# Performance work log

Hardware: AMD Instinct MI355X
Metric: run time of the kernel (lower is better)

The kernel has to match this reference:

```python
import jax, jax.numpy as jnp
import numpy as np

N_NODES = 50000
N_EDGES = 600000
N_FEAT = 64
D = 128
N_GRAPHS = 1024
N_LAYERS = 4


def setup_inputs() -> dict:
    key = jax.random.key(0)
    ks = jax.random.split(key, 16)
    x = jax.random.normal(ks[0], (N_NODES, N_FEAT), dtype=jnp.float32)
    edge_index = jax.random.randint(ks[1], (2, N_EDGES), 0, N_NODES, dtype=jnp.int64)
    batch_index = jnp.sort(jax.random.randint(ks[2], (N_NODES,), 0, N_GRAPHS, dtype=jnp.int64))
    def lin(k, fan_in, fan_out):
        s = 1.0 / np.sqrt(fan_in)
        kw, kb = jax.random.split(k)
        w = jax.random.uniform(kw, (fan_in, fan_out), minval=-s, maxval=s, dtype=jnp.float32)
        b = jax.random.uniform(kb, (fan_out,), minval=-s, maxval=s, dtype=jnp.float32)
        return w, b
    w0, b0 = lin(ks[3], N_FEAT, D)
    w1, b1 = lin(ks[4], D, D)
    w2, b2 = lin(ks[5], D, D)
    w3, b3 = lin(ks[6], D, D)
    wp, bp = lin(ks[7], D, D)
    return {"x": x, "edge_index": edge_index, "batch_index": batch_index,
            "w0": w0, "b0": b0, "w1": w1, "b1": b1, "w2": w2, "b2": b2,
            "w3": w3, "b3": b3, "wp": wp, "bp": bp}


def _gin_layer(x, src, dst, w, b):
    # GINConv with eps=0: MLP(x_i + sum_{j in N(i)} x_j); MLP = Linear -> ReLU
    agg = jax.ops.segment_sum(x[src], dst, num_segments=N_NODES)
    return jax.nn.relu((x + agg) @ w + b)


def reference(x, edge_index, batch_index, w0, b0, w1, b1, w2, b2, w3, b3, wp, bp):
    src, dst = edge_index[0], edge_index[1]
    # first layer changes width 64 -> 128; agg happens in input width
    agg0 = jax.ops.segment_sum(x[src], dst, num_segments=N_NODES)
    h = jax.nn.relu((x + agg0) @ w0 + b0)
    for w, b in ((w1, b1), (w2, b2), (w3, b3)):
        h = _gin_layer(h, src, dst, w, b)
    # global mean pool per graph
    sums = jax.ops.segment_sum(h, batch_index, num_segments=N_GRAPHS)
    counts = jax.ops.segment_sum(jnp.ones((N_NODES,), dtype=h.dtype), batch_index, num_segments=N_GRAPHS)
    pooled = sums / jnp.maximum(counts, 1.0)[:, None]
    # post_mp: Linear -> ReLU (dropout identity at inference)
    return jax.nn.relu(pooled @ wp + bp)
```

## Files before the change

kernel.cpp:

```cpp
#include <hip/hip_runtime.h>
#include <hip/hip_fp16.h>


#define N_NODES  50000
#define N_EDGES  600000
#define N_FEAT   64
#define DIM      128
#define N_GRAPHS 1024
#define NB_SCAN  49

typedef _Float16 f16x8 __attribute__((ext_vector_type(8)));
typedef float    f32x4 __attribute__((ext_vector_type(4)));

__global__ __launch_bounds__(256) void hist_k(
    const int* __restrict__ dst, int* __restrict__ cnt) {
  int e = blockIdx.x * 256 + threadIdx.x;
  if (e < N_EDGES) atomicAdd(&cnt[dst[e]], 1);
}

__global__ __launch_bounds__(256) void scan_part_k(
    const int* __restrict__ cnt, int* __restrict__ part) {
  __shared__ int ws[4];
  int t = threadIdx.x, b = blockIdx.x;
  int base = b * 1024 + t * 4;
  int s = 0;
  if (base + 3 < N_NODES) {
    int4 v = *reinterpret_cast<const int4*>(cnt + base);
    s = v.x + v.y + v.z + v.w;
  } else {
    for (int i = 0; i < 4; ++i) if (base + i < N_NODES) s += cnt[base + i];
  }
  for (int off = 32; off; off >>= 1) s += __shfl_down(s, off, 64);
  int lane = t & 63, wv = t >> 6;
  if (lane == 0) ws[wv] = s;
  __syncthreads();
  if (t == 0) part[b] = ws[0] + ws[1] + ws[2] + ws[3];
}

__global__ __launch_bounds__(256) void scan_write_k(
    const int* __restrict__ cnt, const int* __restrict__ part,
    int* __restrict__ row_ptr, int* __restrict__ fill) {
  __shared__ int wsum[4];
  __shared__ int blk_off_s;
  int t = threadIdx.x, b = blockIdx.x;
  int lane = t & 63, wv = t >> 6;
  int base = b * 1024 + t * 4;

  if (base + 3 < N_NODES)
    *reinterpret_cast<int4*>(fill + base) = make_int4(0, 0, 0, 0);
  else
    for (int i = 0; i < 4; ++i) if (base + i < N_NODES) fill[base + i] = 0;

  if (t < 64) {
    int v = (t < NB_SCAN) ? part[t] : 0;
    int incl = v;
    for (int off = 1; off < 64; off <<= 1) {
      int u = __shfl_up(incl, off, 64);
      if (t >= off) incl += u;
    }
    if (t == b) blk_off_s = incl - v;
  }

  int v[4];
#pragma unroll
  for (int i = 0; i < 4; ++i) v[i] = (base + i < N_NODES) ? cnt[base + i] : 0;
  int ls = v[0] + v[1] + v[2] + v[3];
  int incl = ls;
  for (int off = 1; off < 64; off <<= 1) {
    int u = __shfl_up(incl, off, 64);
    if (lane >= off) incl += u;
  }
  if (lane == 63) wsum[wv] = incl;
  __syncthreads();
  int woff = 0;
  for (int w = 0; w < wv; ++w) woff += wsum[w];
  int off0 = blk_off_s + woff + (incl - ls);
  int rp0 = off0, rp1 = off0 + v[0], rp2 = rp1 + v[1], rp3 = rp2 + v[2];
  if (base + 3 < N_NODES)
    *reinterpret_cast<int4*>(row_ptr + base) = make_int4(rp0, rp1, rp2, rp3);
  else {
    int rp[4] = {rp0, rp1, rp2, rp3};
    for (int i = 0; i < 4; ++i) if (base + i < N_NODES) row_ptr[base + i] = rp[i];
  }
  if (b == 0 && t == 0) row_ptr[N_NODES] = N_EDGES;
}

__global__ __launch_bounds__(256) void fill_k(
    const int* __restrict__ src, const int* __restrict__ dst,
    const int* __restrict__ row_ptr, int* __restrict__ fill,
    int* __restrict__ csr_src) {
  int e = blockIdx.x * 256 + threadIdx.x;
  if (e >= N_EDGES) return;
  int d = dst[e];
  int pos = row_ptr[d] + atomicAdd(&fill[d], 1);
  csr_src[pos] = src[e];
}

#define CNTZ  (N_NODES / 4)
#define XWORK (N_NODES * N_FEAT / 4)
__global__ __launch_bounds__(256) void prep_k(
    const float* __restrict__ x, __half* __restrict__ xh,
    const float* __restrict__ w0, const float* __restrict__ w1,
    const float* __restrict__ w2, const float* __restrict__ w3,
    __half* __restrict__ Wt0, __half* __restrict__ Wt1,
    __half* __restrict__ Wt2, __half* __restrict__ Wt3,
    int* __restrict__ cnt) {
  int i = blockIdx.x * 256 + threadIdx.x;
  if (i < CNTZ) {
    *reinterpret_cast<int4*>(cnt + i * 4) = make_int4(0, 0, 0, 0);
    return;
  }
  i -= CNTZ;
  if (i < XWORK) {
    float4 v = *reinterpret_cast<const float4*>(x + (size_t)i * 4);
    union { __half2 h2[2]; uint2 u; } pk;
    pk.h2[0] = __floats2half2_rn(v.x, v.y);
    pk.h2[1] = __floats2half2_rn(v.z, v.w);
    *reinterpret_cast<uint2*>(xh + (size_t)i * 4) = pk.u;
    return;
  }
  int j = i - XWORK;
  if (j < N_FEAT * DIM) {
    int k = j >> 7, n = j & 127;
    Wt0[n * N_FEAT + k] = __float2half(w0[j]);
    return;
  }
  j -= N_FEAT * DIM;
  if (j >= 3 * DIM * DIM) return;
  int wsel = j / (DIM * DIM);
  int jj = j - wsel * (DIM * DIM);
  int k = jj >> 7, n = jj & 127;
  const float* W = (wsel == 0) ? w1 : (wsel == 1) ? w2 : w3;
  __half* Wt     = (wsel == 0) ? Wt1 : (wsel == 1) ? Wt2 : Wt3;
  Wt[n * DIM + k] = __float2half(W[jj]);
}

template<int K, bool EPI>
__global__ __launch_bounds__(256) void mfma_gemm_k(
    const __half* __restrict__ A, const __half* __restrict__ Wt,
    const float* __restrict__ bias, __half* __restrict__ y, int M) {
  constexpr int KP = K + 8;
  constexpr int OSP = 128 + 16;
  constexpr size_t STAGE = (size_t)(64 + 128) * KP * sizeof(__half);
  constexpr size_t OUTSZ = (size_t)64 * OSP * sizeof(__half);
  __shared__ __align__(16) char smem[STAGE > OUTSZ ? STAGE : OUTSZ];
  __half (*As)[KP]  = reinterpret_cast<__half(*)[KP]>(smem);
  __half (*Ws)[KP]  = reinterpret_cast<__half(*)[KP]>(smem + (size_t)64 * KP * sizeof(__half));
  __half (*Os)[OSP] = reinterpret_cast<__half(*)[OSP]>(smem);

  int tid = threadIdx.x;
  int row0 = blockIdx.x * 64;

  for (int i = tid; i < 64 * (K / 8); i += 256) {
    int r = i / (K / 8), c = (i % (K / 8)) * 8;
    int row = row0 + r;
    f16x8 v = {};
    if (row < M) v = *reinterpret_cast<const f16x8*>(A + (size_t)row * K + c);
    *reinterpret_cast<f16x8*>(&As[r][c]) = v;
  }
  for (int i = tid; i < 128 * (K / 8); i += 256) {
    int r = i / (K / 8), c = (i % (K / 8)) * 8;
    *reinterpret_cast<f16x8*>(&Ws[r][c]) =
        *reinterpret_cast<const f16x8*>(Wt + (size_t)r * K + c);
  }
  __syncthreads();

  int w = tid >> 6, lane = tid & 63;
  int quad = lane >> 4, m = lane & 15;

  f32x4 acc[8];
#pragma unroll
  for (int t = 0; t < 8; ++t) acc[t] = (f32x4){0.f, 0.f, 0.f, 0.f};

#pragma unroll
  for (int kk = 0; kk < K; kk += 32) {
    f16x8 a = *reinterpret_cast<const f16x8*>(&As[w * 16 + m][kk + quad * 8]);
#pragma unroll
    for (int t = 0; t < 8; ++t) {
      f16x8 b = *reinterpret_cast<const f16x8*>(&Ws[t * 16 + m][kk + quad * 8]);
      acc[t] = __builtin_amdgcn_mfma_f32_16x16x32_f16(a, b, acc[t], 0, 0, 0);
    }
  }

  __syncthreads();

#pragma unroll
  for (int t = 0; t < 8; ++t) {
    float bv = EPI ? bias[t * 16 + m] : 0.f;
#pragma unroll
    for (int r = 0; r < 4; ++r) {
      float v = acc[t][r];
      if (EPI) v = fmaxf(v + bv, 0.f);
      Os[w * 16 + quad * 4 + r][t * 16 + m] = __float2half(v);
    }
  }
  __syncthreads();

#pragma unroll
  for (int it = 0; it < 4; ++it) {
    int i = tid + it * 256;
    int r = i >> 4, c = (i & 15) * 8;
    int row = row0 + r;
    if (row < M)
      *reinterpret_cast<f16x8*>(y + (size_t)row * 128 + c) =
          *reinterpret_cast<const f16x8*>(&Os[r][c]);
  }
}

template<int F, bool BR>
__global__ __launch_bounds__(256) void gather_k(
    const __half* __restrict__ y, const int* __restrict__ row_ptr,
    const int* __restrict__ csr_src, const float* __restrict__ bias,
    __half* __restrict__ hout) {
  constexpr int CH = F / 8;
  const f16x8* yv = reinterpret_cast<const f16x8*>(y);
  int gid  = blockIdx.x * 256 + threadIdx.x;
  int node = gid / CH;
  int l    = gid % CH;
  if (node >= N_NODES) return;
  int beg = row_ptr[node], end = row_ptr[node + 1];

  f16x8 self = yv[(size_t)node * CH + l];
  float acc[8];
#pragma unroll
  for (int v = 0; v < 8; ++v) acc[v] = (float)self[v];

  int e = beg;
  for (; e + 3 < end; e += 4) {
    int s0 = csr_src[e+0], s1 = csr_src[e+1], s2 = csr_src[e+2], s3 = csr_src[e+3];
    f16x8 v0 = yv[(size_t)s0 * CH + l];
    f16x8 v1 = yv[(size_t)s1 * CH + l];
    f16x8 v2 = yv[(size_t)s2 * CH + l];
    f16x8 v3 = yv[(size_t)s3 * CH + l];
#pragma unroll
    for (int v = 0; v < 8; ++v)
      acc[v] += ((float)v0[v] + (float)v1[v]) + ((float)v2[v] + (float)v3[v]);
  }
  for (; e < end; ++e) {
    f16x8 v0 = yv[(size_t)csr_src[e] * CH + l];
#pragma unroll
    for (int v = 0; v < 8; ++v) acc[v] += (float)v0[v];
  }

  f16x8 o;
  if (BR) {
    float4 b0 = *reinterpret_cast<const float4*>(bias + l * 8);
    float4 b1 = *reinterpret_cast<const float4*>(bias + l * 8 + 4);
    float bb[8] = {b0.x, b0.y, b0.z, b0.w, b1.x, b1.y, b1.z, b1.w};
#pragma unroll
    for (int v = 0; v < 8; ++v) o[v] = (_Float16)fmaxf(acc[v] + bb[v], 0.f);
  } else {
#pragma unroll
    for (int v = 0; v < 8; ++v) o[v] = (_Float16)acc[v];
  }
  reinterpret_cast<f16x8*>(hout)[(size_t)node * CH + l] = o;
}

__global__ __launch_bounds__(128) void pool_post_k(
    const __half* __restrict__ h, const int* __restrict__ batch,
    const float* __restrict__ W, const float* __restrict__ bias,
    float* __restrict__ out) {
  __shared__ float xs[DIM];
  int g = blockIdx.x;
  int col = threadIdx.x;
  int lo = 0, hi = N_NODES;
  while (lo < hi) { int mid = (lo + hi) >> 1; if (batch[mid] < g) lo = mid + 1; else hi = mid; }
  int beg = lo;
  hi = N_NODES;
  while (lo < hi) { int mid = (lo + hi) >> 1; if (batch[mid] < g + 1) lo = mid + 1; else hi = mid; }
  int end = lo;

  float acc = 0.f;
  for (int n = beg; n < end; ++n) acc += __half2float(h[(size_t)n * DIM + col]);
  float cnt = fmaxf((float)(end - beg), 1.0f);
  xs[col] = acc / cnt;
  __syncthreads();
  float o = bias[col];
  for (int k = 0; k < DIM; ++k)
    o = fmaf(xs[k], W[(size_t)k * DIM + col], o);
  out[(size_t)g * DIM + col] = fmaxf(o, 0.f);
}

extern "C" void kernel_launch(void* const* d_in, const int* in_sizes, int n_in,
                              void* d_out, int out_size, void* d_ws, size_t ws_size,
                              hipStream_t stream) {
  const float* x    = (const float*)d_in[0];
  const int*   ei   = (const int*)d_in[1];
  const int*   batch= (const int*)d_in[2];
  const float* w0 = (const float*)d_in[3];  const float* b0 = (const float*)d_in[4];
  const float* w1 = (const float*)d_in[5];  const float* b1 = (const float*)d_in[6];
  const float* w2 = (const float*)d_in[7];  const float* b2 = (const float*)d_in[8];
  const float* w3 = (const float*)d_in[9];  const float* b3 = (const float*)d_in[10];
  const float* wp = (const float*)d_in[11]; const float* bp = (const float*)d_in[12];
  float* out = (float*)d_out;

  const int* src = ei;
  const int* dst = ei + N_EDGES;

  __half* xh = (__half*)d_ws;
  __half* y  = xh + (size_t)N_NODES * N_FEAT;
  __half* h  = y  + (size_t)N_NODES * DIM;
  __half* Wt0 = h + (size_t)N_NODES * DIM;
  __half* Wt1 = Wt0 + N_FEAT * DIM;
  __half* Wt2 = Wt1 + DIM * DIM;
  __half* Wt3 = Wt2 + DIM * DIM;
  int* cnt     = (int*)(Wt3 + DIM * DIM);
  int* fill    = cnt + N_NODES;
  int* part    = fill + N_NODES;
  int* row_ptr = part + 64;
  int* csr_src = row_ptr + (N_NODES + 1);
  __half* s = y;

  {
    int total = CNTZ + XWORK + N_FEAT * DIM + 3 * DIM * DIM;
    prep_k<<<(total + 255) / 256, 256, 0, stream>>>(x, xh, w0, w1, w2, w3,
                                                    Wt0, Wt1, Wt2, Wt3, cnt);
  }
  hist_k<<<(N_EDGES + 255) / 256, 256, 0, stream>>>(dst, cnt);
  scan_part_k <<<NB_SCAN, 256, 0, stream>>>(cnt, part);
  scan_write_k<<<NB_SCAN, 256, 0, stream>>>(cnt, part, row_ptr, fill);
  fill_k<<<(N_EDGES + 255) / 256, 256, 0, stream>>>(src, dst, row_ptr, fill, csr_src);

  int mgrid = (N_NODES + 63) / 64;

  gather_k<N_FEAT, false><<<(N_NODES * (N_FEAT/8) + 255) / 256, 256, 0, stream>>>(
      xh, row_ptr, csr_src, nullptr, s);
  mfma_gemm_k<N_FEAT, true><<<mgrid, 256, 0, stream>>>(s, Wt0, b0, h, N_NODES);

  const __half* Wl[3] = {Wt1, Wt2, Wt3};
  const float*  Bl[3] = {b1, b2, b3};
  for (int l = 0; l < 3; ++l) {
    mfma_gemm_k<DIM, false><<<mgrid, 256, 0, stream>>>(h, Wl[l], nullptr, y, N_NODES);
    gather_k<DIM, true><<<(N_NODES * (DIM/8) + 255) / 256, 256, 0, stream>>>(
        y, row_ptr, csr_src, Bl[l], h);
  }

  pool_post_k<<<N_GRAPHS, 128, 0, stream>>>(h, batch, wp, bp, out);
}
```

Measured before the change: 311.7 us.

## Fuse all GNN stages into one persistent cooperative kernel with grid syncs

Replaces the chain of about fifteen separate kernel launches with a single cooperative persistent kernel of 512 blocks that runs each stage as a grid-stride phase, separated by grid-wide barriers, to remove launch overhead and inter-kernel gaps. The GEMM is also retiled to 128-row tiles, with A fragments held in registers and two MFMA row-slabs per wave. A multi-kernel fallback path is kept for devices that cannot do cooperative launch. The cost is limited parallelism per phase (a fixed 512-block grid) and grid.sync overhead, and the pool phase now runs on 256-thread blocks with half the threads idle.

```diff
diff --git a/kernel.cpp b/kernel.cpp
--- a/kernel.cpp
+++ b/kernel.cpp
@@ -1,5 +1,8 @@
 #include <hip/hip_runtime.h>
 #include <hip/hip_fp16.h>
+#include <hip/hip_cooperative_groups.h>
+
+namespace cg = cooperative_groups;
 
 
 #define N_NODES  50000
@@ -8,62 +11,113 @@
 #define DIM      128
 #define N_GRAPHS 1024
 #define NB_SCAN  49
+#define GRID     512
+#define TPB      256
+#define GT128    ((N_NODES + 127) / 128)
+#define SMEM_BYTES 36864
 
 typedef _Float16 f16x8 __attribute__((ext_vector_type(8)));
 typedef float    f32x4 __attribute__((ext_vector_type(4)));
 
-__global__ __launch_bounds__(256) void hist_k(
-    const int* __restrict__ dst, int* __restrict__ cnt) {
-  int e = blockIdx.x * 256 + threadIdx.x;
-  if (e < N_EDGES) atomicAdd(&cnt[dst[e]], 1);
-}
-
-__global__ __launch_bounds__(256) void scan_part_k(
-    const int* __restrict__ cnt, int* __restrict__ part) {
-  __shared__ int ws[4];
-  int t = threadIdx.x, b = blockIdx.x;
+#define CNTZ  (N_NODES / 4)
+#define XWORK (N_NODES * N_FEAT / 4)
+#define PREP_TOTAL (CNTZ + XWORK + N_FEAT * DIM + 3 * DIM * DIM)
+
+struct Params {
+  const float* x; const int* src; const int* dst; const int* batch;
+  const float *w0, *b0, *w1, *b1, *w2, *b2, *w3, *b3, *wp, *bp;
+  float* out;
+  __half *xh, *y, *h, *Wt0, *Wt1, *Wt2, *Wt3;
+  int *cnt, *fill, *part, *row_ptr, *csr_src;
+};
+
+
+__device__ __forceinline__ void prep_phase(const Params& p) {
+  for (int i0 = blockIdx.x * TPB + threadIdx.x; i0 < PREP_TOTAL;
+       i0 += gridDim.x * TPB) {
+    int i = i0;
+    if (i < CNTZ) {
+      *reinterpret_cast<int4*>(p.cnt + i * 4) = make_int4(0, 0, 0, 0);
+      continue;
+    }
+    i -= CNTZ;
+    if (i < XWORK) {
+      float4 v = *reinterpret_cast<const float4*>(p.x + (size_t)i * 4);
+      union { __half2 h2[2]; uint2 u; } pk;
+      pk.h2[0] = __floats2half2_rn(v.x, v.y);
+      pk.h2[1] = __floats2half2_rn(v.z, v.w);
+      *reinterpret_cast<uint2*>(p.xh + (size_t)i * 4) = pk.u;
+      continue;
+    }
+    int j = i - XWORK;
+    if (j < N_FEAT * DIM) {
+      int k = j >> 7, n = j & 127;
+      p.Wt0[n * N_FEAT + k] = __float2half(p.w0[j]);
+      continue;
+    }
+    j -= N_FEAT * DIM;
+    int wsel = j / (DIM * DIM);
+    int jj = j - wsel * (DIM * DIM);
+    int k = jj >> 7, n = jj & 127;
+    const float* W = (wsel == 0) ? p.w1 : (wsel == 1) ? p.w2 : p.w3;
+    __half* Wt     = (wsel == 0) ? p.Wt1 : (wsel == 1) ? p.Wt2 : p.Wt3;
+    Wt[n * DIM + k] = __float2half(W[jj]);
+  }
+}
+
+__device__ __forceinline__ void hist_phase(const Params& p) {
+  for (int e = blockIdx.x * TPB + threadIdx.x; e < N_EDGES;
+       e += gridDim.x * TPB)
+    atomicAdd(&p.cnt[p.dst[e]], 1);
+}
+
+__device__ __forceinline__ void scan_part_phase(const Params& p, char* smem) {
+  int b = blockIdx.x;
+  if (b >= NB_SCAN) return;
+  int* ws = reinterpret_cast<int*>(smem);
+  int t = threadIdx.x;
   int base = b * 1024 + t * 4;
   int s = 0;
   if (base + 3 < N_NODES) {
-    int4 v = *reinterpret_cast<const int4*>(cnt + base);
+    int4 v = *reinterpret_cast<const int4*>(p.cnt + base);
     s = v.x + v.y + v.z + v.w;
   } else {
-    for (int i = 0; i < 4; ++i) if (base + i < N_NODES) s += cnt[base + i];
+    for (int i = 0; i < 4; ++i) if (base + i < N_NODES) s += p.cnt[base + i];
   }
   for (int off = 32; off; off >>= 1) s += __shfl_down(s, off, 64);
   int lane = t & 63, wv = t >> 6;
   if (lane == 0) ws[wv] = s;
   __syncthreads();
-  if (t == 0) part[b] = ws[0] + ws[1] + ws[2] + ws[3];
-}
-
-__global__ __launch_bounds__(256) void scan_write_k(
-    const int* __restrict__ cnt, const int* __restrict__ part,
-    int* __restrict__ row_ptr, int* __restrict__ fill) {
-  __shared__ int wsum[4];
-  __shared__ int blk_off_s;
-  int t = threadIdx.x, b = blockIdx.x;
+  if (t == 0) p.part[b] = ws[0] + ws[1] + ws[2] + ws[3];
+}
+
+__device__ __forceinline__ void scan_write_phase(const Params& p, char* smem) {
+  int b = blockIdx.x;
+  if (b >= NB_SCAN) return;
+  int* wsum = reinterpret_cast<int*>(smem);
+  int* blk_off_s = reinterpret_cast<int*>(smem) + 4;
+  int t = threadIdx.x;
   int lane = t & 63, wv = t >> 6;
   int base = b * 1024 + t * 4;
 
   if (base + 3 < N_NODES)
-    *reinterpret_cast<int4*>(fill + base) = make_int4(0, 0, 0, 0);
+    *reinterpret_cast<int4*>(p.fill + base) = make_int4(0, 0, 0, 0);
   else
-    for (int i = 0; i < 4; ++i) if (base + i < N_NODES) fill[base + i] = 0;
+    for (int i = 0; i < 4; ++i) if (base + i < N_NODES) p.fill[base + i] = 0;
 
   if (t < 64) {
-    int v = (t < NB_SCAN) ? part[t] : 0;
+    int v = (t < NB_SCAN) ? p.part[t] : 0;
     int incl = v;
     for (int off = 1; off < 64; off <<= 1) {
       int u = __shfl_up(incl, off, 64);
       if (t >= off) incl += u;
     }
-    if (t == b) blk_off_s = incl - v;
+    if (t == b) *blk_off_s = incl - v;
   }
 
   int v[4];
 #pragma unroll
-  for (int i = 0; i < 4; ++i) v[i] = (base + i < N_NODES) ? cnt[base + i] : 0;
+  for (int i = 0; i < 4; ++i) v[i] = (base + i < N_NODES) ? p.cnt[base + i] : 0;
   int ls = v[0] + v[1] + v[2] + v[3];
   int incl = ls;
   for (int off = 1; off < 64; off <<= 1) {
@@ -74,266 +128,294 @@
   __syncthreads();
   int woff = 0;
   for (int w = 0; w < wv; ++w) woff += wsum[w];
-  int off0 = blk_off_s + woff + (incl - ls);
+  int off0 = *blk_off_s + woff + (incl - ls);
   int rp0 = off0, rp1 = off0 + v[0], rp2 = rp1 + v[1], rp3 = rp2 + v[2];
   if (base + 3 < N_NODES)
-    *reinterpret_cast<int4*>(row_ptr + base) = make_int4(rp0, rp1, rp2, rp3);
+    *reinterpret_cast<int4*>(p.row_ptr + base) = make_int4(rp0, rp1, rp2, rp3);
   else {
     int rp[4] = {rp0, rp1, rp2, rp3};
-    for (int i = 0; i < 4; ++i) if (base + i < N_NODES) row_ptr[base + i] = rp[i];
-  }
-  if (b == 0 && t == 0) row_ptr[N_NODES] = N_EDGES;
-}
-
-__global__ __launch_bounds__(256) void fill_k(
-    const int* __restrict__ src, const int* __restrict__ dst,
-    const int* __restrict__ row_ptr, int* __restrict__ fill,
-    int* __restrict__ csr_src) {
-  int e = blockIdx.x * 256 + threadIdx.x;
-  if (e >= N_EDGES) return;
-  int d = dst[e];
-  int pos = row_ptr[d] + atomicAdd(&fill[d], 1);
-  csr_src[pos] = src[e];
-}
-
-#define CNTZ  (N_NODES / 4)
-#define XWORK (N_NODES * N_FEAT / 4)
-__global__ __launch_bounds__(256) void prep_k(
-    const float* __restrict__ x, __half* __restrict__ xh,
-    const float* __restrict__ w0, const float* __restrict__ w1,
-    const float* __restrict__ w2, const float* __restrict__ w3,
-    __half* __restrict__ Wt0, __half* __restrict__ Wt1,
-    __half* __restrict__ Wt2, __half* __restrict__ Wt3,
-    int* __restrict__ cnt) {
-  int i = blockIdx.x * 256 + threadIdx.x;
-  if (i < CNTZ) {
-    *reinterpret_cast<int4*>(cnt + i * 4) = make_int4(0, 0, 0, 0);
-    return;
-  }
-  i -= CNTZ;
-  if (i < XWORK) {
-    float4 v = *reinterpret_cast<const float4*>(x + (size_t)i * 4);
-    union { __half2 h2[2]; uint2 u; } pk;
-    pk.h2[0] = __floats2half2_rn(v.x, v.y);
-    pk.h2[1] = __floats2half2_rn(v.z, v.w);
-    *reinterpret_cast<uint2*>(xh + (size_t)i * 4) = pk.u;
-    return;
-  }
-  int j = i - XWORK;
-  if (j < N_FEAT * DIM) {
-    int k = j >> 7, n = j & 127;
-    Wt0[n * N_FEAT + k] = __float2half(w0[j]);
-    return;
-  }
-  j -= N_FEAT * DIM;
-  if (j >= 3 * DIM * DIM) return;
-  int wsel = j / (DIM * DIM);
-  int jj = j - wsel * (DIM * DIM);
-  int k = jj >> 7, n = jj & 127;
-  const float* W = (wsel == 0) ? w1 : (wsel == 1) ? w2 : w3;
-  __half* Wt     = (wsel == 0) ? Wt1 : (wsel == 1) ? Wt2 : Wt3;
-  Wt[n * DIM + k] = __float2half(W[jj]);
+    for (int i = 0; i < 4; ++i) if (base + i < N_NODES) p.row_ptr[base + i] = rp[i];
+  }
+  if (b == 0 && t == 0) p.row_ptr[N_NODES] = N_EDGES;
+}
+
+__device__ __forceinline__ void fill_phase(const Params& p) {
+  for (int e = blockIdx.x * TPB + threadIdx.x; e < N_EDGES;
+       e += gridDim.x * TPB) {
+    int d = p.dst[e];
+    int pos = p.row_ptr[d] + atomicAdd(&p.fill[d], 1);
+    p.csr_src[pos] = p.src[e];
+  }
+}
+
+template<int F, bool BR>
+__device__ __forceinline__ void gather_phase(
+    const __half* yIn, const float* bias, __half* hout, const Params& p) {
+  constexpr int CH = F / 8;
+  const f16x8* yv = reinterpret_cast<const f16x8*>(yIn);
+  for (int gid = blockIdx.x * TPB + threadIdx.x; gid < N_NODES * CH;
+       gid += gridDim.x * TPB) {
+    int node = gid / CH;
+    int l    = gid % CH;
+    int beg = p.row_ptr[node], end = p.row_ptr[node + 1];
+
+    f16x8 self = yv[(size_t)node * CH + l];
+    float acc[8];
+#pragma unroll
+    for (int v = 0; v < 8; ++v) acc[v] = (float)self[v];
+
+    int e = beg;
+    for (; e + 3 < end; e += 4) {
+      int s0 = p.csr_src[e+0], s1 = p.csr_src[e+1];
+      int s2 = p.csr_src[e+2], s3 = p.csr_src[e+3];
+      f16x8 v0 = yv[(size_t)s0 * CH + l];
+      f16x8 v1 = yv[(size_t)s1 * CH + l];
+      f16x8 v2 = yv[(size_t)s2 * CH + l];
+      f16x8 v3 = yv[(size_t)s3 * CH + l];
+#pragma unroll
+      for (int v = 0; v < 8; ++v)
+        acc[v] += ((float)v0[v] + (float)v1[v]) + ((float)v2[v] + (float)v3[v]);
+    }
+    for (; e < end; ++e) {
+      f16x8 v0 = yv[(size_t)p.csr_src[e] * CH + l];
+#pragma unroll
+      for (int v = 0; v < 8; ++v) acc[v] += (float)v0[v];
+    }
+
+    f16x8 o;
+    if (BR) {
+      float4 b0 = *reinterpret_cast<const float4*>(bias + l * 8);
+      float4 b1 = *reinterpret_cast<const float4*>(bias + l * 8 + 4);
+      float bb[8] = {b0.x, b0.y, b0.z, b0.w, b1.x, b1.y, b1.z, b1.w};
+#pragma unroll
+      for (int v = 0; v < 8; ++v) o[v] = (_Float16)fmaxf(acc[v] + bb[v], 0.f);
+    } else {
+#pragma unroll
+      for (int v = 0; v < 8; ++v) o[v] = (_Float16)acc[v];
+    }
+    reinterpret_cast<f16x8*>(hout)[(size_t)node * CH + l] = o;
+  }
 }
 
 template<int K, bool EPI>
-__global__ __launch_bounds__(256) void mfma_gemm_k(
-    const __half* __restrict__ A, const __half* __restrict__ Wt,
-    const float* __restrict__ bias, __half* __restrict__ y, int M) {
+__device__ __forceinline__ void gemm_phase(
+    const __half* A, const __half* Wt, const float* bias, __half* yOut,
+    char* smem) {
   constexpr int KP = K + 8;
-  constexpr int OSP = 128 + 16;
-  constexpr size_t STAGE = (size_t)(64 + 128) * KP * sizeof(__half);
-  constexpr size_t OUTSZ = (size_t)64 * OSP * sizeof(__half);
-  __shared__ __align__(16) char smem[STAGE > OUTSZ ? STAGE : OUTSZ];
-  __half (*As)[KP]  = reinterpret_cast<__half(*)[KP]>(smem);
-  __half (*Ws)[KP]  = reinterpret_cast<__half(*)[KP]>(smem + (size_t)64 * KP * sizeof(__half));
+  constexpr int OSP = 144;
+  constexpr int NKC = K / 32;
+  __half (*Ws)[KP]  = reinterpret_cast<__half(*)[KP]>(smem);
   __half (*Os)[OSP] = reinterpret_cast<__half(*)[OSP]>(smem);
 
   int tid = threadIdx.x;
-  int row0 = blockIdx.x * 64;
-
-  for (int i = tid; i < 64 * (K / 8); i += 256) {
-    int r = i / (K / 8), c = (i % (K / 8)) * 8;
-    int row = row0 + r;
-    f16x8 v = {};
-    if (row < M) v = *reinterpret_cast<const f16x8*>(A + (size_t)row * K + c);
-    *reinterpret_cast<f16x8*>(&As[r][c]) = v;
-  }
-  for (int i = tid; i < 128 * (K / 8); i += 256) {
-    int r = i / (K / 8), c = (i % (K / 8)) * 8;
-    *reinterpret_cast<f16x8*>(&Ws[r][c]) =
-        *reinterpret_cast<const f16x8*>(Wt + (size_t)r * K + c);
-  }
-  __syncthreads();
-
   int w = tid >> 6, lane = tid & 63;
   int quad = lane >> 4, m = lane & 15;
 
-  f32x4 acc[8];
-#pragma unroll
-  for (int t = 0; t < 8; ++t) acc[t] = (f32x4){0.f, 0.f, 0.f, 0.f};
-
-#pragma unroll
-  for (int kk = 0; kk < K; kk += 32) {
-    f16x8 a = *reinterpret_cast<const f16x8*>(&As[w * 16 + m][kk + quad * 8]);
+  for (int tile = blockIdx.x; tile < GT128; tile += gridDim.x) {
+    int row0 = tile * 128;
+
+    for (int i = tid; i < 128 * (K / 8); i += TPB) {
+      int r = i / (K / 8), c = (i % (K / 8)) * 8;
+      *reinterpret_cast<f16x8*>(&Ws[r][c]) =
+          *reinterpret_cast<const f16x8*>(Wt + (size_t)r * K + c);
+    }
+
+    f16x8 areg[2][NKC];
+#pragma unroll
+    for (int s = 0; s < 2; ++s) {
+      int row = row0 + w * 32 + s * 16 + m;
+      row = min(row, N_NODES - 1);
+      const f16x8* Ar = reinterpret_cast<const f16x8*>(A + (size_t)row * K);
+#pragma unroll
+      for (int kc = 0; kc < NKC; ++kc)
+        areg[s][kc] = Ar[kc * 4 + quad];
+    }
+    __syncthreads();
+
+    f32x4 acc[2][8];
+#pragma unroll
+    for (int s = 0; s < 2; ++s)
+#pragma unroll
+      for (int t = 0; t < 8; ++t) acc[s][t] = (f32x4){0.f, 0.f, 0.f, 0.f};
+
+#pragma unroll
+    for (int kc = 0; kc < NKC; ++kc) {
+#pragma unroll
+      for (int t = 0; t < 8; ++t) {
+        f16x8 b = *reinterpret_cast<const f16x8*>(&Ws[t * 16 + m][kc * 32 + quad * 8]);
+        acc[0][t] = __builtin_amdgcn_mfma_f32_16x16x32_f16(areg[0][kc], b, acc[0][t], 0, 0, 0);
+        acc[1][t] = __builtin_amdgcn_mfma_f32_16x16x32_f16(areg[1][kc], b, acc[1][t], 0, 0, 0);
+      }
+    }
+
+    __syncthreads();
+
 #pragma unroll
     for (int t = 0; t < 8; ++t) {
-      f16x8 b = *reinterpret_cast<const f16x8*>(&Ws[t * 16 + m][kk + quad * 8]);
-      acc[t] = __builtin_amdgcn_mfma_f32_16x16x32_f16(a, b, acc[t], 0, 0, 0);
-    }
-  }
-
-  __syncthreads();
-
-#pragma unroll
-  for (int t = 0; t < 8; ++t) {
-    float bv = EPI ? bias[t * 16 + m] : 0.f;
-#pragma unroll
-    for (int r = 0; r < 4; ++r) {
-      float v = acc[t][r];
-      if (EPI) v = fmaxf(v + bv, 0.f);
-      Os[w * 16 + quad * 4 + r][t * 16 + m] = __float2half(v);
-    }
-  }
-  __syncthreads();
-
-#pragma unroll
-  for (int it = 0; it < 4; ++it) {
-    int i = tid + it * 256;
-    int r = i >> 4, c = (i & 15) * 8;
-    int row = row0 + r;
-    if (row < M)
-      *reinterpret_cast<f16x8*>(y + (size_t)row * 128 + c) =
-          *reinterpret_cast<const f16x8*>(&Os[r][c]);
-  }
-}
-
+      float bv = EPI ? bias[t * 16 + m] : 0.f;
+#pragma unroll
+      for (int s = 0; s < 2; ++s)
+#pragma unroll
+        for (int r = 0; r < 4; ++r) {
+          float v = acc[s][t][r];
+          if (EPI) v = fmaxf(v + bv, 0.f);
+          Os[w * 32 + s * 16 + quad * 4 + r][t * 16 + m] = __float2half(v);
+        }
+    }
+    __syncthreads();
+
+#pragma unroll
+    for (int it = 0; it < 8; ++it) {
+      int i = tid + it * TPB;
+      int r = i >> 4, c = (i & 15) * 8;
+      int row = row0 + r;
+      if (row < N_NODES)
+        *reinterpret_cast<f16x8*>(yOut + (size_t)row * 128 + c) =
+            *reinterpret_cast<const f16x8*>(&Os[r][c]);
+    }
+    __syncthreads();
+  }
+}
+
+__device__ __forceinline__ void pool_phase(const Params& p, char* smem) {
+  float* xs = reinterpret_cast<float*>(smem);
+  int col = threadIdx.x;
+  for (int g = blockIdx.x; g < N_GRAPHS; g += gridDim.x) {
+    int lo = 0, hi = N_NODES;
+    while (lo < hi) { int mid = (lo + hi) >> 1; if (p.batch[mid] < g) lo = mid + 1; else hi = mid; }
+    int beg = lo;
+    hi = N_NODES;
+    while (lo < hi) { int mid = (lo + hi) >> 1; if (p.batch[mid] < g + 1) lo = mid + 1; else hi = mid; }
+    int end = lo;
+
+    if (col < DIM) {
+      float acc = 0.f;
+      for (int n = beg; n < end; ++n) acc += __half2float(p.h[(size_t)n * DIM + col]);
+      float cnt = fmaxf((float)(end - beg), 1.0f);
+      xs[col] = acc / cnt;
+    }
+    __syncthreads();
+    if (col < DIM) {
+      float o = p.bp[col];
+      for (int k = 0; k < DIM; ++k)
+        o = fmaf(xs[k], p.wp[(size_t)k * DIM + col], o);
+      p.out[(size_t)g * DIM + col] = fmaxf(o, 0.f);
+    }
+    __syncthreads();
+  }
+}
+
+__global__ __launch_bounds__(TPB, 2) void gin_all_k(Params p) {
+  cg::grid_group grid = cg::this_grid();
+  __shared__ __align__(16) char smem[SMEM_BYTES];
+
+  prep_phase(p);                                          grid.sync();
+  hist_phase(p);                                          grid.sync();
+  scan_part_phase(p, smem);                               grid.sync();
+  scan_write_phase(p, smem);                              grid.sync();
+  fill_phase(p);                                          grid.sync();
+
+  gather_phase<N_FEAT, false>(p.xh, nullptr, p.y, p);     grid.sync();
+  gemm_phase<N_FEAT, true>(p.y, p.Wt0, p.b0, p.h, smem);  grid.sync();
+
+  gemm_phase<DIM, false>(p.h, p.Wt1, nullptr, p.y, smem); grid.sync();
+  gather_phase<DIM, true>(p.y, p.b1, p.h, p);             grid.sync();
+  gemm_phase<DIM, false>(p.h, p.Wt2, nullptr, p.y, smem); grid.sync();
+  gather_phase<DIM, true>(p.y, p.b2, p.h, p);             grid.sync();
+  gemm_phase<DIM, false>(p.h, p.Wt3, nullptr, p.y, smem); grid.sync();
+  gather_phase<DIM, true>(p.y, p.b3, p.h, p);             grid.sync();
+
+  pool_phase(p, smem);
+}
+
+__global__ __launch_bounds__(TPB) void prep_w(Params p)       { prep_phase(p); }
+__global__ __launch_bounds__(TPB) void hist_w(Params p)       { hist_phase(p); }
+__global__ __launch_bounds__(TPB) void scan_part_w(Params p)  {
+  __shared__ __align__(16) char smem[64]; scan_part_phase(p, smem); }
+__global__ __launch_bounds__(TPB) void scan_write_w(Params p) {
+  __shared__ __align__(16) char smem[64]; scan_write_phase(p, smem); }
+__global__ __launch_bounds__(TPB) void fill_w(Params p)       { fill_phase(p); }
 template<int F, bool BR>
-__global__ __launch_bounds__(256) void gather_k(
-    const __half* __restrict__ y, const int* __restrict__ row_ptr,
-    const int* __restrict__ csr_src, const float* __restrict__ bias,
-    __half* __restrict__ hout) {
-  constexpr int CH = F / 8;
-  const f16x8* yv = reinterpret_cast<const f16x8*>(y);
-  int gid  = blockIdx.x * 256 + threadIdx.x;
-  int node = gid / CH;
-  int l    = gid % CH;
-  if (node >= N_NODES) return;
-  int beg = row_ptr[node], end = row_ptr[node + 1];
-
-  f16x8 self = yv[(size_t)node * CH + l];
-  float acc[8];
-#pragma unroll
-  for (int v = 0; v < 8; ++v) acc[v] = (float)self[v];
-
-  int e = beg;
-  for (; e + 3 < end; e += 4) {
-    int s0 = csr_src[e+0], s1 = csr_src[e+1], s2 = csr_src[e+2], s3 = csr_src[e+3];
-    f16x8 v0 = yv[(size_t)s0 * CH + l];
-    f16x8 v1 = yv[(size_t)s1 * CH + l];
-    f16x8 v2 = yv[(size_t)s2 * CH + l];
-    f16x8 v3 = yv[(size_t)s3 * CH + l];
-#pragma unroll
-    for (int v = 0; v < 8; ++v)
-      acc[v] += ((float)v0[v] + (float)v1[v]) + ((float)v2[v] + (float)v3[v]);
-  }
-  for (; e < end; ++e) {
-    f16x8 v0 = yv[(size_t)csr_src[e] * CH + l];
-#pragma unroll
-    for (int v = 0; v < 8; ++v) acc[v] += (float)v0[v];
-  }
-
-  f16x8 o;
-  if (BR) {
-    float4 b0 = *reinterpret_cast<const float4*>(bias + l * 8);
-    float4 b1 = *reinterpret_cast<const float4*>(bias + l * 8 + 4);
-    float bb[8] = {b0.x, b0.y, b0.z, b0.w, b1.x, b1.y, b1.z, b1.w};
-#pragma unroll
-    for (int v = 0; v < 8; ++v) o[v] = (_Float16)fmaxf(acc[v] + bb[v], 0.f);
-  } else {
-#pragma unroll
-    for (int v = 0; v < 8; ++v) o[v] = (_Float16)acc[v];
-  }
-  reinterpret_cast<f16x8*>(hout)[(size_t)node * CH + l] = o;
-}
-
-__global__ __launch_bounds__(128) void pool_post_k(
-    const __half* __restrict__ h, const int* __restrict__ batch,
-    const float* __restrict__ W, const float* __restrict__ bias,
-    float* __restrict__ out) {
-  __shared__ float xs[DIM];
-  int g = blockIdx.x;
-  int col = threadIdx.x;
-  int lo = 0, hi = N_NODES;
-  while (lo < hi) { int mid = (lo + hi) >> 1; if (batch[mid] < g) lo = mid + 1; else hi = mid; }
-  int beg = lo;
-  hi = N_NODES;
-  while (lo < hi) { int mid = (lo + hi) >> 1; if (batch[mid] < g + 1) lo = mid + 1; else hi = mid; }
-  int end = lo;
-
-  float acc = 0.f;
-  for (int n = beg; n < end; ++n) acc += __half2float(h[(size_t)n * DIM + col]);
-  float cnt = fmaxf((float)(end - beg), 1.0f);
-  xs[col] = acc / cnt;
-  __syncthreads();
-  float o = bias[col];
-  for (int k = 0; k < DIM; ++k)
-    o = fmaf(xs[k], W[(size_t)k * DIM + col], o);
-  out[(size_t)g * DIM + col] = fmaxf(o, 0.f);
+__global__ __launch_bounds__(TPB) void gather_w(Params p, const __half* yIn,
+                                                const float* bias, __half* hout) {
+  gather_phase<F, BR>(yIn, bias, hout, p);
+}
+template<int K, bool EPI>
+__global__ __launch_bounds__(TPB) void gemm_w(Params p, const __half* A,
+                                              const __half* Wt,
+                                              const float* bias, __half* yOut) {
+  __shared__ __align__(16) char smem[SMEM_BYTES];
+  gemm_phase<K, EPI>(A, Wt, bias, yOut, smem);
+}
+__global__ __launch_bounds__(TPB) void pool_w(Params p) {
+  __shared__ __align__(16) char smem[DIM * sizeof(float)];
+  pool_phase(p, smem);
+}
+
+static void run_fallback(const Params& p, hipStream_t stream) {
+  prep_w<<<(PREP_TOTAL + TPB - 1) / TPB, TPB, 0, stream>>>(p);
+  hist_w<<<(N_EDGES + TPB - 1) / TPB, TPB, 0, stream>>>(p);
+  scan_part_w<<<NB_SCAN, TPB, 0, stream>>>(p);
+  scan_write_w<<<NB_SCAN, TPB, 0, stream>>>(p);
+  fill_w<<<(N_EDGES + TPB - 1) / TPB, TPB, 0, stream>>>(p);
+
+  gather_w<N_FEAT, false><<<(N_NODES * 8 + TPB - 1) / TPB, TPB, 0, stream>>>(
+      p, p.xh, nullptr, p.y);
+  gemm_w<N_FEAT, true><<<GT128, TPB, 0, stream>>>(p, p.y, p.Wt0, p.b0, p.h);
+
+  const __half* Wl[3] = {p.Wt1, p.Wt2, p.Wt3};
+  const float*  Bl[3] = {p.b1, p.b2, p.b3};
+  for (int l = 0; l < 3; ++l) {
+    gemm_w<DIM, false><<<GT128, TPB, 0, stream>>>(p, p.h, Wl[l], nullptr, p.y);
+    gather_w<DIM, true><<<(N_NODES * 16 + TPB - 1) / TPB, TPB, 0, stream>>>(
+        p, p.y, Bl[l], p.h);
+  }
+  pool_w<<<N_GRAPHS, TPB, 0, stream>>>(p);
 }
 
 extern "C" void kernel_launch(void* const* d_in, const int* in_sizes, int n_in,
                               void* d_out, int out_size, void* d_ws, size_t ws_size,
                               hipStream_t stream) {
-  const float* x    = (const float*)d_in[0];
-  const int*   ei   = (const int*)d_in[1];
-  const int*   batch= (const int*)d_in[2];
-  const float* w0 = (const float*)d_in[3];  const float* b0 = (const float*)d_in[4];
-  const float* w1 = (const float*)d_in[5];  const float* b1 = (const float*)d_in[6];
-  const float* w2 = (const float*)d_in[7];  const float* b2 = (const float*)d_in[8];
-  const float* w3 = (const float*)d_in[9];  const float* b3 = (const float*)d_in[10];
-  const float* wp = (const float*)d_in[11]; const float* bp = (const float*)d_in[12];
-  float* out = (float*)d_out;
-
-  const int* src = ei;
-  const int* dst = ei + N_EDGES;
-
-  __half* xh = (__half*)d_ws;
-  __half* y  = xh + (size_t)N_NODES * N_FEAT;
-  __half* h  = y  + (size_t)N_NODES * DIM;
-  __half* Wt0 = h + (size_t)N_NODES * DIM;
-  __half* Wt1 = Wt0 + N_FEAT * DIM;
-  __half* Wt2 = Wt1 + DIM * DIM;
-  __half* Wt3 = Wt2 + DIM * DIM;
-  int* cnt     = (int*)(Wt3 + DIM * DIM);
-  int* fill    = cnt + N_NODES;
-  int* part    = fill + N_NODES;
-  int* row_ptr = part + 64;
-  int* csr_src = row_ptr + (N_NODES + 1);
-  __half* s = y;
-
-  {
-    int total = CNTZ + XWORK + N_FEAT * DIM + 3 * DIM * DIM;
-    prep_k<<<(total + 255) / 256, 256, 0, stream>>>(x, xh, w0, w1, w2, w3,
-                                                    Wt0, Wt1, Wt2, Wt3, cnt);
-  }
-  hist_k<<<(N_EDGES + 255) / 256, 256, 0, stream>>>(dst, cnt);
-  scan_part_k <<<NB_SCAN, 256, 0, stream>>>(cnt, part);
-  scan_write_k<<<NB_SCAN, 256, 0, stream>>>(cnt, part, row_ptr, fill);
-  fill_k<<<(N_EDGES + 255) / 256, 256, 0, stream>>>(src, dst, row_ptr, fill, csr_src);
-
-  int mgrid = (N_NODES + 63) / 64;
-
-  gather_k<N_FEAT, false><<<(N_NODES * (N_FEAT/8) + 255) / 256, 256, 0, stream>>>(
-      xh, row_ptr, csr_src, nullptr, s);
-  mfma_gemm_k<N_FEAT, true><<<mgrid, 256, 0, stream>>>(s, Wt0, b0, h, N_NODES);
-
-  const __half* Wl[3] = {Wt1, Wt2, Wt3};
-  const float*  Bl[3] = {b1, b2, b3};
-  for (int l = 0; l < 3; ++l) {
-    mfma_gemm_k<DIM, false><<<mgrid, 256, 0, stream>>>(h, Wl[l], nullptr, y, N_NODES);
-    gather_k<DIM, true><<<(N_NODES * (DIM/8) + 255) / 256, 256, 0, stream>>>(
-        y, row_ptr, csr_src, Bl[l], h);
-  }
-
-  pool_post_k<<<N_GRAPHS, 128, 0, stream>>>(h, batch, wp, bp, out);
-}
+  Params p;
+  p.x     = (const float*)d_in[0];
+  const int* ei = (const int*)d_in[1];
+  p.src   = ei;
+  p.dst   = ei + N_EDGES;
+  p.batch = (const int*)d_in[2];
+  p.w0 = (const float*)d_in[3];  p.b0 = (const float*)d_in[4];
+  p.w1 = (const float*)d_in[5];  p.b1 = (const float*)d_in[6];
+  p.w2 = (const float*)d_in[7];  p.b2 = (const float*)d_in[8];
+  p.w3 = (const float*)d_in[9];  p.b3 = (const float*)d_in[10];
+  p.wp = (const float*)d_in[11]; p.bp = (const float*)d_in[12];
+  p.out = (float*)d_out;
+
+  p.xh  = (__half*)d_ws;
+  p.y   = p.xh + (size_t)N_NODES * N_FEAT;
+  p.h   = p.y  + (size_t)N_NODES * DIM;
+  p.Wt0 = p.h  + (size_t)N_NODES * DIM;
+  p.Wt1 = p.Wt0 + N_FEAT * DIM;
+  p.Wt2 = p.Wt1 + DIM * DIM;
+  p.Wt3 = p.Wt2 + DIM * DIM;
+  p.cnt     = (int*)(p.Wt3 + DIM * DIM);
+  p.fill    = p.cnt + N_NODES;
+  p.part    = p.fill + N_NODES;
+  p.row_ptr = p.part + 64;
+  p.csr_src = p.row_ptr + (N_NODES + 1);
+
+  int dev = 0;
+  hipGetDevice(&dev);
+  int coop = 0, ncu = 0, nb = 0;
+  hipDeviceGetAttribute(&coop, hipDeviceAttributeCooperativeLaunch, dev);
+  hipDeviceGetAttribute(&ncu, hipDeviceAttributeMultiprocessorCount, dev);
+  hipOccupancyMaxActiveBlocksPerMultiprocessor(&nb, (const void*)gin_all_k,
+                                               TPB, 0);
+  bool use_coop = coop && ((long)nb * ncu >= GRID);
+
+  if (use_coop) {
+    void* args[] = {&p};
+    hipError_t err = hipLaunchCooperativeKernel((void*)gin_all_k, dim3(GRID),
+                                                dim3(TPB), args, 0, stream);
+    if (err == hipSuccess) return;
+  }
+  run_fallback(p, stream);
+}
```

After: 306.9 us. Within noise of the previous version (-1.5%).

## Sort nodes by in-degree for gather load balance and enlarge GEMM tiles

Applied to the files above, without the earlier changes.

Bins nodes by in-degree during the scan kernels and builds a node_order permutation, so gather threads in the same wavefront process nodes with similar edge counts and diverge less. Separately, the GEMM now handles 128 rows per block, with A fragments loaded straight into registers and each B fragment reused for two MFMAs. The costs are extra atomics and writes in the scan kernels, an indirect node lookup in gather, and scattered writes to the output h, whose rows are no longer written in order.

```diff
diff --git a/kernel.cpp b/kernel.cpp
--- a/kernel.cpp
+++ b/kernel.cpp
@@ -8,40 +8,98 @@
 #define DIM      128
 #define N_GRAPHS 1024
 #define NB_SCAN  49
+#define NBINS    36
+#define TPB      256
+#define GT128    ((N_NODES + 127) / 128)
 
 typedef _Float16 f16x8 __attribute__((ext_vector_type(8)));
 typedef float    f32x4 __attribute__((ext_vector_type(4)));
 
-__global__ __launch_bounds__(256) void hist_k(
+#define CNTZ  (N_NODES / 4)
+#define XWORK (N_NODES * N_FEAT / 4)
+#define PREP_TOTAL (CNTZ + XWORK + N_FEAT * DIM + 3 * DIM * DIM)
+
+__global__ __launch_bounds__(TPB) void prep_k(
+    const float* __restrict__ x, __half* __restrict__ xh,
+    const float* __restrict__ w0, const float* __restrict__ w1,
+    const float* __restrict__ w2, const float* __restrict__ w3,
+    __half* __restrict__ Wt0, __half* __restrict__ Wt1,
+    __half* __restrict__ Wt2, __half* __restrict__ Wt3,
+    int* __restrict__ cnt) {
+  int i = blockIdx.x * TPB + threadIdx.x;
+  if (i < CNTZ) {
+    *reinterpret_cast<int4*>(cnt + i * 4) = make_int4(0, 0, 0, 0);
+    return;
+  }
+  i -= CNTZ;
+  if (i < XWORK) {
+    float4 v = *reinterpret_cast<const float4*>(x + (size_t)i * 4);
+    union { __half2 h2[2]; uint2 u; } pk;
+    pk.h2[0] = __floats2half2_rn(v.x, v.y);
+    pk.h2[1] = __floats2half2_rn(v.z, v.w);
+    *reinterpret_cast<uint2*>(xh + (size_t)i * 4) = pk.u;
+    return;
+  }
+  int j = i - XWORK;
+  if (j < N_FEAT * DIM) {
+    int k = j >> 7, n = j & 127;
+    Wt0[n * N_FEAT + k] = __float2half(w0[j]);
+    return;
+  }
+  j -= N_FEAT * DIM;
+  if (j >= 3 * DIM * DIM) return;
+  int wsel = j / (DIM * DIM);
+  int jj = j - wsel * (DIM * DIM);
+  int k = jj >> 7, n = jj & 127;
+  const float* W = (wsel == 0) ? w1 : (wsel == 1) ? w2 : w3;
+  __half* Wt     = (wsel == 0) ? Wt1 : (wsel == 1) ? Wt2 : Wt3;
+  Wt[n * DIM + k] = __float2half(W[jj]);
+}
+
+__global__ __launch_bounds__(TPB) void hist_k(
     const int* __restrict__ dst, int* __restrict__ cnt) {
-  int e = blockIdx.x * 256 + threadIdx.x;
+  int e = blockIdx.x * TPB + threadIdx.x;
   if (e < N_EDGES) atomicAdd(&cnt[dst[e]], 1);
 }
 
-__global__ __launch_bounds__(256) void scan_part_k(
-    const int* __restrict__ cnt, int* __restrict__ part) {
+__global__ __launch_bounds__(TPB) void scan_part_k(
+    const int* __restrict__ cnt, int* __restrict__ part,
+    int* __restrict__ bins) {
   __shared__ int ws[4];
+  __shared__ int lbin[NBINS];
   int t = threadIdx.x, b = blockIdx.x;
+  if (t < NBINS) lbin[t] = 0;
+  __syncthreads();
   int base = b * 1024 + t * 4;
   int s = 0;
+  int v[4] = {0, 0, 0, 0};
   if (base + 3 < N_NODES) {
-    int4 v = *reinterpret_cast<const int4*>(cnt + base);
-    s = v.x + v.y + v.z + v.w;
+    int4 q = *reinterpret_cast<const int4*>(cnt + base);
+    v[0] = q.x; v[1] = q.y; v[2] = q.z; v[3] = q.w;
   } else {
-    for (int i = 0; i < 4; ++i) if (base + i < N_NODES) s += cnt[base + i];
+    for (int i = 0; i < 4; ++i) if (base + i < N_NODES) v[i] = cnt[base + i];
+  }
+#pragma unroll
+  for (int i = 0; i < 4; ++i) {
+    s += v[i];
+    if (base + i < N_NODES) atomicAdd(&lbin[min(v[i], NBINS - 1)], 1);
   }
   for (int off = 32; off; off >>= 1) s += __shfl_down(s, off, 64);
   int lane = t & 63, wv = t >> 6;
   if (lane == 0) ws[wv] = s;
   __syncthreads();
   if (t == 0) part[b] = ws[0] + ws[1] + ws[2] + ws[3];
-}
-
-__global__ __launch_bounds__(256) void scan_write_k(
+  if (t < NBINS) bins[b * NBINS + t] = lbin[t];
+}
+
+__global__ __launch_bounds__(TPB) void scan_write_k(
     const int* __restrict__ cnt, const int* __restrict__ part,
-    int* __restrict__ row_ptr, int* __restrict__ fill) {
+    const int* __restrict__ bins, int* __restrict__ row_ptr,
+    int* __restrict__ fill, int* __restrict__ node_order) {
   __shared__ int wsum[4];
   __shared__ int blk_off_s;
+  __shared__ int offj[NBINS];
+  __shared__ int lrank[NBINS];
   int t = threadIdx.x, b = blockIdx.x;
   int lane = t & 63, wv = t >> 6;
   int base = b * 1024 + t * 4;
@@ -60,6 +118,25 @@
     }
     if (t == b) blk_off_s = incl - v;
   }
+
+  int colbelow = 0, coltot = 0;
+  if (t < NBINS) {
+    for (int b2 = 0; b2 < NB_SCAN; ++b2) {
+      int u = bins[b2 * NBINS + t];
+      if (b2 < b) colbelow += u;
+      coltot += u;
+    }
+  }
+  if (t < 64) {
+    int v = (t < NBINS) ? coltot : 0;
+    int incl = v;
+    for (int off = 1; off < 64; off <<= 1) {
+      int u = __shfl_up(incl, off, 64);
+      if (t >= off) incl += u;
+    }
+    if (t < NBINS) offj[t] = (incl - v) + colbelow;
+  }
+  if (t < NBINS) lrank[t] = 0;
 
   int v[4];
 #pragma unroll
@@ -83,102 +160,77 @@
     for (int i = 0; i < 4; ++i) if (base + i < N_NODES) row_ptr[base + i] = rp[i];
   }
   if (b == 0 && t == 0) row_ptr[N_NODES] = N_EDGES;
-}
-
-__global__ __launch_bounds__(256) void fill_k(
+
+#pragma unroll
+  for (int i = 0; i < 4; ++i) {
+    if (base + i < N_NODES) {
+      int bin = min(v[i], NBINS - 1);
+      int r = atomicAdd(&lrank[bin], 1);
+      node_order[offj[bin] + r] = base + i;
+    }
+  }
+}
+
+__global__ __launch_bounds__(TPB) void fill_k(
     const int* __restrict__ src, const int* __restrict__ dst,
     const int* __restrict__ row_ptr, int* __restrict__ fill,
     int* __restrict__ csr_src) {
-  int e = blockIdx.x * 256 + threadIdx.x;
+  int e = blockIdx.x * TPB + threadIdx.x;
   if (e >= N_EDGES) return;
   int d = dst[e];
   int pos = row_ptr[d] + atomicAdd(&fill[d], 1);
   csr_src[pos] = src[e];
 }
 
-#define CNTZ  (N_NODES / 4)
-#define XWORK (N_NODES * N_FEAT / 4)
-__global__ __launch_bounds__(256) void prep_k(
-    const float* __restrict__ x, __half* __restrict__ xh,
-    const float* __restrict__ w0, const float* __restrict__ w1,
-    const float* __restrict__ w2, const float* __restrict__ w3,
-    __half* __restrict__ Wt0, __half* __restrict__ Wt1,
-    __half* __restrict__ Wt2, __half* __restrict__ Wt3,
-    int* __restrict__ cnt) {
-  int i = blockIdx.x * 256 + threadIdx.x;
-  if (i < CNTZ) {
-    *reinterpret_cast<int4*>(cnt + i * 4) = make_int4(0, 0, 0, 0);
-    return;
-  }
-  i -= CNTZ;
-  if (i < XWORK) {
-    float4 v = *reinterpret_cast<const float4*>(x + (size_t)i * 4);
-    union { __half2 h2[2]; uint2 u; } pk;
-    pk.h2[0] = __floats2half2_rn(v.x, v.y);
-    pk.h2[1] = __floats2half2_rn(v.z, v.w);
-    *reinterpret_cast<uint2*>(xh + (size_t)i * 4) = pk.u;
-    return;
-  }
-  int j = i - XWORK;
-  if (j < N_FEAT * DIM) {
-    int k = j >> 7, n = j & 127;
-    Wt0[n * N_FEAT + k] = __float2half(w0[j]);
-    return;
-  }
-  j -= N_FEAT * DIM;
-  if (j >= 3 * DIM * DIM) return;
-  int wsel = j / (DIM * DIM);
-  int jj = j - wsel * (DIM * DIM);
-  int k = jj >> 7, n = jj & 127;
-  const float* W = (wsel == 0) ? w1 : (wsel == 1) ? w2 : w3;
-  __half* Wt     = (wsel == 0) ? Wt1 : (wsel == 1) ? Wt2 : Wt3;
-  Wt[n * DIM + k] = __float2half(W[jj]);
-}
-
 template<int K, bool EPI>
-__global__ __launch_bounds__(256) void mfma_gemm_k(
+__global__ __launch_bounds__(TPB) void gemm_k(
     const __half* __restrict__ A, const __half* __restrict__ Wt,
-    const float* __restrict__ bias, __half* __restrict__ y, int M) {
+    const float* __restrict__ bias, __half* __restrict__ y) {
   constexpr int KP = K + 8;
-  constexpr int OSP = 128 + 16;
-  constexpr size_t STAGE = (size_t)(64 + 128) * KP * sizeof(__half);
-  constexpr size_t OUTSZ = (size_t)64 * OSP * sizeof(__half);
-  __shared__ __align__(16) char smem[STAGE > OUTSZ ? STAGE : OUTSZ];
-  __half (*As)[KP]  = reinterpret_cast<__half(*)[KP]>(smem);
-  __half (*Ws)[KP]  = reinterpret_cast<__half(*)[KP]>(smem + (size_t)64 * KP * sizeof(__half));
+  constexpr int OSP = 144;
+  constexpr int NKC = K / 32;
+  constexpr size_t WSZ = (size_t)128 * KP * sizeof(__half);
+  constexpr size_t OSZ = (size_t)128 * OSP * sizeof(__half);
+  __shared__ __align__(16) char smem[WSZ > OSZ ? WSZ : OSZ];
+  __half (*Ws)[KP]  = reinterpret_cast<__half(*)[KP]>(smem);
   __half (*Os)[OSP] = reinterpret_cast<__half(*)[OSP]>(smem);
 
   int tid = threadIdx.x;
-  int row0 = blockIdx.x * 64;
-
-  for (int i = tid; i < 64 * (K / 8); i += 256) {
-    int r = i / (K / 8), c = (i % (K / 8)) * 8;
-    int row = row0 + r;
-    f16x8 v = {};
-    if (row < M) v = *reinterpret_cast<const f16x8*>(A + (size_t)row * K + c);
-    *reinterpret_cast<f16x8*>(&As[r][c]) = v;
-  }
-  for (int i = tid; i < 128 * (K / 8); i += 256) {
+  int w = tid >> 6, lane = tid & 63;
+  int quad = lane >> 4, m = lane & 15;
+  int row0 = blockIdx.x * 128;
+
+  for (int i = tid; i < 128 * (K / 8); i += TPB) {
     int r = i / (K / 8), c = (i % (K / 8)) * 8;
     *reinterpret_cast<f16x8*>(&Ws[r][c]) =
         *reinterpret_cast<const f16x8*>(Wt + (size_t)r * K + c);
   }
-  __syncthreads();
-
-  int w = tid >> 6, lane = tid & 63;
-  int quad = lane >> 4, m = lane & 15;
-
-  f32x4 acc[8];
-#pragma unroll
-  for (int t = 0; t < 8; ++t) acc[t] = (f32x4){0.f, 0.f, 0.f, 0.f};
-
-#pragma unroll
-  for (int kk = 0; kk < K; kk += 32) {
-    f16x8 a = *reinterpret_cast<const f16x8*>(&As[w * 16 + m][kk + quad * 8]);
+
+  f16x8 areg[2][NKC];
+#pragma unroll
+  for (int s = 0; s < 2; ++s) {
+    int row = row0 + w * 32 + s * 16 + m;
+    row = min(row, N_NODES - 1);
+    const f16x8* Ar = reinterpret_cast<const f16x8*>(A + (size_t)row * K);
+#pragma unroll
+    for (int kc = 0; kc < NKC; ++kc)
+      areg[s][kc] = Ar[kc * 4 + quad];
+  }
+  __syncthreads();
+
+  f32x4 acc[2][8];
+#pragma unroll
+  for (int s = 0; s < 2; ++s)
+#pragma unroll
+    for (int t = 0; t < 8; ++t) acc[s][t] = (f32x4){0.f, 0.f, 0.f, 0.f};
+
+#pragma unroll
+  for (int kc = 0; kc < NKC; ++kc) {
 #pragma unroll
     for (int t = 0; t < 8; ++t) {
-      f16x8 b = *reinterpret_cast<const f16x8*>(&Ws[t * 16 + m][kk + quad * 8]);
-      acc[t] = __builtin_amdgcn_mfma_f32_16x16x32_f16(a, b, acc[t], 0, 0, 0);
+      f16x8 b = *reinterpret_cast<const f16x8*>(&Ws[t * 16 + m][kc * 32 + quad * 8]);
+      acc[0][t] = __builtin_amdgcn_mfma_f32_16x16x32_f16(areg[0][kc], b, acc[0][t], 0, 0, 0);
+      acc[1][t] = __builtin_amdgcn_mfma_f32_16x16x32_f16(areg[1][kc], b, acc[1][t], 0, 0, 0);
     }
   }
 
@@ -188,36 +240,39 @@
   for (int t = 0; t < 8; ++t) {
     float bv = EPI ? bias[t * 16 + m] : 0.f;
 #pragma unroll
-    for (int r = 0; r < 4; ++r) {
-      float v = acc[t][r];
-      if (EPI) v = fmaxf(v + bv, 0.f);
-      Os[w * 16 + quad * 4 + r][t * 16 + m] = __float2half(v);
-    }
-  }
-  __syncthreads();
-
-#pragma unroll
-  for (int it = 0; it < 4; ++it) {
-    int i = tid + it * 256;
+    for (int s = 0; s < 2; ++s)
+#pragma unroll
+      for (int r = 0; r < 4; ++r) {
+        float v = acc[s][t][r];
+        if (EPI) v = fmaxf(v + bv, 0.f);
+        Os[w * 32 + s * 16 + quad * 4 + r][t * 16 + m] = __float2half(v);
+      }
+  }
+  __syncthreads();
+
+#pragma unroll
+  for (int it = 0; it < 8; ++it) {
+    int i = tid + it * TPB;
     int r = i >> 4, c = (i & 15) * 8;
     int row = row0 + r;
-    if (row < M)
+    if (row < N_NODES)
       *reinterpret_cast<f16x8*>(y + (size_t)row * 128 + c) =
           *reinterpret_cast<const f16x8*>(&Os[r][c]);
   }
 }
 
 template<int F, bool BR>
-__global__ __launch_bounds__(256) void gather_k(
+__global__ __launch_bounds__(TPB) void gather_k(
     const __half* __restrict__ y, const int* __restrict__ row_ptr,
-    const int* __restrict__ csr_src, const float* __restrict__ bias,
-    __half* __restrict__ hout) {
+    const int* __restrict__ csr_src, const int* __restrict__ order,
+    const float* __restrict__ bias, __half* __restrict__ hout) {
   constexpr int CH = F / 8;
   const f16x8* yv = reinterpret_cast<const f16x8*>(y);
-  int gid  = blockIdx.x * 256 + threadIdx.x;
-  int node = gid / CH;
+  int gid  = blockIdx.x * TPB + threadIdx.x;
+  int rank = gid / CH;
   int l    = gid % CH;
-  if (node >= N_NODES) return;
+  if (rank >= N_NODES) return;
+  int node = order[rank];
   int beg = row_ptr[node], end = row_ptr[node + 1];
 
   f16x8 self = yv[(size_t)node * CH + l];
@@ -309,30 +364,29 @@
   int* part    = fill + N_NODES;
   int* row_ptr = part + 64;
   int* csr_src = row_ptr + (N_NODES + 1);
+  int* node_order = csr_src + N_EDGES;
+  int* bins       = node_order + N_NODES;
   __half* s = y;
 
-  {
-    int total = CNTZ + XWORK + N_FEAT * DIM + 3 * DIM * DIM;
-    prep_k<<<(total + 255) / 256, 256, 0, stream>>>(x, xh, w0, w1, w2, w3,
-                                                    Wt0, Wt1, Wt2, Wt3, cnt);
-  }
-  hist_k<<<(N_EDGES + 255) / 256, 256, 0, stream>>>(dst, cnt);
-  scan_part_k <<<NB_SCAN, 256, 0, stream>>>(cnt, part);
-  scan_write_k<<<NB_SCAN, 256, 0, stream>>>(cnt, part, row_ptr, fill);
-  fill_k<<<(N_EDGES + 255) / 256, 256, 0, stream>>>(src, dst, row_ptr, fill, csr_src);
-
-  int mgrid = (N_NODES + 63) / 64;
-
-  gather_k<N_FEAT, false><<<(N_NODES * (N_FEAT/8) + 255) / 256, 256, 0, stream>>>(
-      xh, row_ptr, csr_src, nullptr, s);
-  mfma_gemm_k<N_FEAT, true><<<mgrid, 256, 0, stream>>>(s, Wt0, b0, h, N_NODES);
+  prep_k<<<(PREP_TOTAL + TPB - 1) / TPB, TPB, 0, stream>>>(
+      x, xh, w0, w1, w2, w3, Wt0, Wt1, Wt2, Wt3, cnt);
+  hist_k<<<(N_EDGES + TPB - 1) / TPB, TPB, 0, stream>>>(dst, cnt);
+  scan_part_k <<<NB_SCAN, TPB, 0, stream>>>(cnt, part, bins);
+  scan_write_k<<<NB_SCAN, TPB, 0, stream>>>(cnt, part, bins, row_ptr, fill,
+                                            node_order);
+  fill_k<<<(N_EDGES + TPB - 1) / TPB, TPB, 0, stream>>>(src, dst, row_ptr,
+                                                        fill, csr_src);
+
+  gather_k<N_FEAT, false><<<(N_NODES * 8 + TPB - 1) / TPB, TPB, 0, stream>>>(
+      xh, row_ptr, csr_src, node_order, nullptr, s);
+  gemm_k<N_FEAT, true><<<GT128, TPB, 0, stream>>>(s, Wt0, b0, h);
 
   const __half* Wl[3] = {Wt1, Wt2, Wt3};
   const float*  Bl[3] = {b1, b2, b3};
   for (int l = 0; l < 3; ++l) {
-    mfma_gemm_k<DIM, false><<<mgrid, 256, 0, stream>>>(h, Wl[l], nullptr, y, N_NODES);
-    gather_k<DIM, true><<<(N_NODES * (DIM/8) + 255) / 256, 256, 0, stream>>>(
-        y, row_ptr, csr_src, Bl[l], h);
+    gemm_k<DIM, false><<<GT128, TPB, 0, stream>>>(h, Wl[l], nullptr, y);
+    gather_k<DIM, true><<<(N_NODES * 16 + TPB - 1) / TPB, TPB, 0, stream>>>(
+        y, row_ptr, csr_src, node_order, Bl[l], h);
   }
 
   pool_post_k<<<N_GRAPHS, 128, 0, stream>>>(h, batch, wp, bp, out);
```

Result: no change. 307.9 us (-1.2%).
